# Kernel tuning notes

Measured on AMD Instinct MI355X. Metric: run time of the kernel, lower is better.

The kernel has to match this reference:

```python
import jax, jax.numpy as jnp
import numpy as np

HIDDEN = 1024
HEADS = 16
HEAD_DIM = HIDDEN // HEADS


def setup_inputs() -> dict:
    key = jax.random.key(0)
    k_x, k_wq, k_bq, k_wo, k_bo = jax.random.split(key, 5)
    x = jax.random.normal(k_x, (2, 2048, HIDDEN), dtype=jnp.float32)
    s = 1.0 / np.sqrt(HIDDEN)
    W_qkv = jax.random.uniform(k_wq, (HIDDEN, 3 * HIDDEN), jnp.float32, -s, s)
    b_qkv = jax.random.uniform(k_bq, (3 * HIDDEN,), jnp.float32, -s, s)
    W_out = jax.random.uniform(k_wo, (HIDDEN, HIDDEN), jnp.float32, -s, s)
    b_out = jax.random.uniform(k_bo, (HIDDEN,), jnp.float32, -s, s)
    return {"x": x, "W_qkv": W_qkv, "b_qkv": b_qkv, "W_out": W_out, "b_out": b_out}


def reference(x, W_qkv, b_qkv, W_out, b_out):
    B, S, D = x.shape
    qkv = x @ W_qkv + b_qkv                       # [B,S,3D]
    qkv = qkv.reshape(B, S, 3, HEADS, HEAD_DIM)
    qkv = jnp.transpose(qkv, (2, 0, 3, 1, 4))     # [3,B,H,S,Dh]
    q, k, v = qkv[0], qkv[1], qkv[2]
    scores = jnp.einsum("bhsd,bhtd->bhst", q, k) / np.sqrt(HEAD_DIM)
    attn = jax.nn.softmax(scores, axis=-1)        # [B,H,S,S]
    out = jnp.einsum("bhst,bhtd->bhsd", attn, v)  # [B,H,S,Dh]
    out = jnp.transpose(out, (0, 2, 1, 3)).reshape(B, S, D)
    return out @ W_out + b_out
```

## Files before the change

kernel.cpp:

```cpp
#include <hip/hip_runtime.h>
#include <hip/hip_bf16.h>

typedef short short8 __attribute__((ext_vector_type(8)));
typedef float float4_ __attribute__((ext_vector_type(4)));
typedef unsigned short ushort_t;
typedef unsigned int uint32_t_;
typedef uint32_t_ uint2v __attribute__((ext_vector_type(2)));
typedef uint32_t_ uint4v __attribute__((ext_vector_type(4)));

#define SCL 0.1803368801111f

__device__ __forceinline__ ushort_t f2bf(float f) {
    uint32_t_ u = __builtin_bit_cast(uint32_t_, f);
    u = (u + 0x7fffu + ((u >> 16) & 1u)) >> 16;
    return (ushort_t)u;
}

__device__ __forceinline__ uint32_t_ pack_bf16(float a, float b) {
    uint32_t_ ua = __builtin_bit_cast(uint32_t_, a) + 0x8000u;
    uint32_t_ ub = __builtin_bit_cast(uint32_t_, b) + 0x8000u;
    return __builtin_amdgcn_perm(ub, ua, 0x07060302);
}

__device__ __forceinline__ uint32_t_ cvt_pk_bf16(float lo, float hi) {
    uint32_t_ r;
    asm("v_cvt_pk_bf16_f32 %0, %1, %2" : "=v"(r) : "v"(lo), "v"(hi));
    return r;
}

#define MFMA32(a, b, c) __builtin_amdgcn_mfma_f32_16x16x32_bf16(a, b, c, 0, 0, 0)

#define GLD_LDS16(g, l) __builtin_amdgcn_global_load_lds( \
    (const __attribute__((address_space(1))) void*)(g),   \
    (__attribute__((address_space(3))) void*)(l), 16, 0, 0)

__global__ __launch_bounds__(256)
void prep_k(const float* __restrict__ x, ushort_t* __restrict__ x_bf,
            const float* __restrict__ Wqkv, ushort_t* __restrict__ WqkvT,
            const float* __restrict__ Wout, ushort_t* __restrict__ WoutT) {
    __shared__ float tile[32][33];
    const int id = blockIdx.x;
    const int tid = threadIdx.x;
    if (id < 4096) {
        int i = (id * 256 + tid) * 4;
        float4 v = *(const float4*)(x + i);
        uint32_t_ lo = (uint32_t_)f2bf(v.x) | ((uint32_t_)f2bf(v.y) << 16);
        uint32_t_ hi = (uint32_t_)f2bf(v.z) | ((uint32_t_)f2bf(v.w) << 16);
        *(uint2*)(x_bf + i) = make_uint2(lo, hi);
        return;
    }
    const float* in;
    ushort_t* out;
    int N, K, n0, k0;
    if (id < 7168) {
        int t = id - 4096;
        in = Wqkv; out = WqkvT; N = 3072; K = 1024;
        n0 = (t % 96) * 32; k0 = (t / 96) * 32;
    } else {
        int t = id - 7168;
        in = Wout; out = WoutT; N = 1024; K = 1024;
        n0 = (t & 31) * 32; k0 = (t >> 5) * 32;
    }
    int tx = tid & 31, ty = tid >> 5;
    #pragma unroll
    for (int i = 0; i < 32; i += 8)
        tile[ty + i][tx] = in[(size_t)(k0 + ty + i) * N + n0 + tx];
    __syncthreads();
    #pragma unroll
    for (int i = 0; i < 32; i += 8)
        out[(size_t)(n0 + ty + i) * K + k0 + tx] = f2bf(tile[tx][ty + i]);
}

template <int TN, bool QKV_EPI>
__global__ __launch_bounds__(256, TN == 128 ? 3 : 4)
void gemm_dbuf_k(const ushort_t* __restrict__ A, const ushort_t* __restrict__ Bt,
                 const float* __restrict__ bias, void* __restrict__ C,
                 ushort_t* __restrict__ Vt_out, int M, int N, int K) {
    constexpr int NB   = TN / 32;
    constexpr int SETB = 8192 + TN * 64;
    __shared__ char smem[2 * SETB];
    const int tid  = threadIdx.x;
    const int m0   = blockIdx.y * 128;
    const int n0   = blockIdx.x * TN;
    const int w    = tid >> 6;
    const int lane = tid & 63;
    const int wm   = (w >> 1) * 64;
    const int wn   = (w & 1) * (TN / 2);
    const int quad = lane >> 4;
    const int l16  = lane & 15;

    const int sr = 16 * w + (lane >> 2);
    const int sc = ((lane & 3) ^ ((sr >> 1) & 3)) * 8;
    const ushort_t* ag0 = A  + (size_t)(m0 + sr) * K + sc;
    const ushort_t* ag1 = A  + (size_t)(m0 + sr + 64) * K + sc;
    const ushort_t* bg0 = Bt + (size_t)(n0 + sr) * K + sc;
    const ushort_t* bg1 = Bt + (size_t)(n0 + sr + 64) * K + sc;
    char* sA = smem + 1024 * w;
    char* sB = smem + 8192 + 1024 * w;

    int aoff[4], boff[NB];
    #pragma unroll
    for (int i = 0; i < 4; i++) {
        int row = wm + i * 16 + l16;
        aoff[i] = row * 64 + ((quad ^ ((row >> 1) & 3)) * 16);
    }
    #pragma unroll
    for (int i = 0; i < NB; i++) {
        int row = wn + i * 16 + l16;
        boff[i] = 8192 + row * 64 + ((quad ^ ((row >> 1) & 3)) * 16);
    }

    float4_ acc[4][NB] = {};
    const int NIT = K >> 5;

    GLD_LDS16(ag0, sA);
    GLD_LDS16(ag1, sA + 4096);
    GLD_LDS16(bg0, sB);
    if (TN == 128) GLD_LDS16(bg1, sB + 4096);

    for (int it = 0; it < NIT; ++it) {
        __syncthreads();
        if (it + 1 < NIT) {
            const int nk = (it + 1) * 32;
            char* dA = sA + ((it + 1) & 1) * SETB;
            char* dB = sB + ((it + 1) & 1) * SETB;
            GLD_LDS16(ag0 + nk, dA);
            GLD_LDS16(ag1 + nk, dA + 4096);
            GLD_LDS16(bg0 + nk, dB);
            if (TN == 128) GLD_LDS16(bg1 + nk, dB + 4096);
        }
        const char* base = smem + (it & 1) * SETB;
        short8 af[4], bf[NB];
        #pragma unroll
        for (int i = 0; i < 4; i++)  af[i] = *(const short8*)(base + aoff[i]);
        #pragma unroll
        for (int i = 0; i < NB; i++) bf[i] = *(const short8*)(base + boff[i]);
        #pragma unroll
        for (int mi = 0; mi < 4; mi++)
            #pragma unroll
            for (int ni = 0; ni < NB; ni++)
                acc[mi][ni] = MFMA32(af[mi], bf[ni], acc[mi][ni]);
    }

    #pragma unroll
    for (int mi = 0; mi < 4; mi++) {
        int row = m0 + wm + mi * 16 + quad * 4;
        #pragma unroll
        for (int ni = 0; ni < NB; ni++) {
            int col = n0 + wn + ni * 16 + l16;
            float bb = bias[col];
            if (QKV_EPI) {
                if (col < 2048) {
                    float sc2 = (col < 1024) ? SCL : 1.0f;
                    #pragma unroll
                    for (int r = 0; r < 4; r++)
                        ((ushort_t*)C)[(size_t)(row + r) * 2048 + col] =
                            f2bf((acc[mi][ni][r] + bb) * sc2);
                } else {
                    int s0v  = row & 2047;
                    int spos = (s0v & ~31) | (quad << 3) | ((mi & 1) << 2);
                    size_t vrow = (size_t)((row >> 11) * 1024 + (col - 2048));
                    float v0 = acc[mi][ni][0] + bb, v1 = acc[mi][ni][1] + bb;
                    float v2 = acc[mi][ni][2] + bb, v3 = acc[mi][ni][3] + bb;
                    uint2v pk;
                    pk.x = pack_bf16(v0, v1);
                    pk.y = pack_bf16(v2, v3);
                    *(uint2v*)(Vt_out + vrow * 2048 + spos) = pk;
                }
            } else {
                #pragma unroll
                for (int r = 0; r < 4; r++)
                    ((float*)C)[(size_t)(row + r) * N + col] = acc[mi][ni][r] + bb;
            }
        }
    }
}

__global__ __launch_bounds__(256, 4)
void flash_attn_k(const ushort_t* __restrict__ qk, const ushort_t* __restrict__ vt,
                  ushort_t* __restrict__ out) {
    __shared__ char smem[32768];
    const int bh = blockIdx.x;
    const int b  = bh >> 4, h = bh & 15;
    const int q0 = blockIdx.y * 64;
    const int tid  = threadIdx.x;
    const int w    = tid >> 6;
    const int lane = tid & 63;
    const int quad = lane >> 4;
    const int l16  = lane & 15;
    const int qh   = w >> 1;
    const int kh   = w & 1;
    const size_t tok0 = (size_t)b * 2048;
    const int hq = h * 64;

    const int r0 = 16 * w + (lane >> 3), r1 = r0 + 8;
    const int s7 = lane & 7;
    const int c0 = (s7 ^ ((r0 >> 1) & 7)) * 8;
    const int c1 = (s7 ^ ((r1 >> 1) & 7)) * 8;
    const ushort_t* qg0 = qk + (tok0 + q0 + r0) * 2048 + hq + c0;
    const ushort_t* qg1 = qk + (tok0 + q0 + r1) * 2048 + hq + c1;
    const ushort_t* kg0 = qk + (tok0 + r0) * 2048 + 1024 + hq + c0;
    const ushort_t* kg1 = qk + (tok0 + r1) * 2048 + 1024 + hq + c1;
    const ushort_t* vg0 = vt + (size_t)(bh * 64 + r0) * 2048 + c0;
    const ushort_t* vg1 = vt + (size_t)(bh * 64 + r1) * 2048 + c1;
    char* stK = smem + 2048 * w;
    char* stV = smem + 8192 + 2048 * w;
    char* stQ = smem + 16384 + 2048 * w;

    GLD_LDS16(qg0, stQ);
    GLD_LDS16(qg1, stQ + 1024);
    GLD_LDS16(kg0, stK);
    GLD_LDS16(kg1, stK + 1024);
    GLD_LDS16(vg0, stV);
    GLD_LDS16(vg1, stV + 1024);
    __syncthreads();

    const int sw = (l16 >> 1) & 7;
    short8 qf[2][2];
    #pragma unroll
    for (int sub = 0; sub < 2; sub++)
        #pragma unroll
        for (int kk = 0; kk < 2; kk++) {
            int row = qh * 32 + sub * 16 + l16;
            qf[sub][kk] = *(const short8*)(smem + 16384 + row * 128 +
                                           (((kk * 4 + quad) ^ sw) * 16));
        }

    int koff[2][2], voff[4];
    #pragma unroll
    for (int mi = 0; mi < 2; mi++)
        #pragma unroll
        for (int kk = 0; kk < 2; kk++) {
            int row = kh * 32 + mi * 16 + l16;
            koff[mi][kk] = row * 128 + (((kk * 4 + quad) ^ sw) * 16);
        }
    #pragma unroll
    for (int di = 0; di < 4; di++) {
        int row = di * 16 + l16;
        voff[di] = 8192 + row * 128 + (((kh * 4 + quad) ^ sw) * 16);
    }

    float4_ ot[2][4] = {};
    float lsum[2] = {0.f, 0.f};
    short8 vprev[4];
    short8 bpprev[2];

    {
        __syncthreads();
        GLD_LDS16(kg0 + (size_t)64 * 2048, stK + 16384);
        GLD_LDS16(kg1 + (size_t)64 * 2048, stK + 16384 + 1024);
        GLD_LDS16(vg0 + 64, stV + 16384);
        GLD_LDS16(vg1 + 64, stV + 16384 + 1024);
        const char* base = smem;
        float4_ st[2][2];
        #pragma unroll
        for (int mi = 0; mi < 2; mi++) {
            short8 kf0 = *(const short8*)(base + koff[mi][0]);
            short8 kf1 = *(const short8*)(base + koff[mi][1]);
            #pragma unroll
            for (int sub = 0; sub < 2; sub++) {
                float4_ z = {0.f, 0.f, 0.f, 0.f};
                z = MFMA32(kf0, qf[sub][0], z);
                z = MFMA32(kf1, qf[sub][1], z);
                st[mi][sub] = z;
            }
        }
        #pragma unroll
        for (int di = 0; di < 4; di++)
            vprev[di] = *(const short8*)(base + voff[di]);
        #pragma unroll
        for (int sub = 0; sub < 2; sub++) {
            uint4v u;
            #pragma unroll
            for (int mi = 0; mi < 2; mi++) {
                float p0 = __builtin_amdgcn_exp2f(st[mi][sub][0]);
                float p1 = __builtin_amdgcn_exp2f(st[mi][sub][1]);
                float p2 = __builtin_amdgcn_exp2f(st[mi][sub][2]);
                float p3 = __builtin_amdgcn_exp2f(st[mi][sub][3]);
                lsum[sub] += (p0 + p1) + (p2 + p3);
                if (mi == 0) { u.x = cvt_pk_bf16(p0, p1); u.y = cvt_pk_bf16(p2, p3); }
                else         { u.z = cvt_pk_bf16(p0, p1); u.w = cvt_pk_bf16(p2, p3); }
            }
            bpprev[sub] = __builtin_bit_cast(short8, u);
        }
    }

    for (int kt = 64; kt < 2048; kt += 64) {
        __syncthreads();
        const int set = (kt >> 6) & 1;
        if (kt + 64 < 2048) {
            const int nb = (set ^ 1) * 16384;
            const size_t go = (size_t)(kt + 64);
            GLD_LDS16(kg0 + go * 2048, stK + nb);
            GLD_LDS16(kg1 + go * 2048, stK + nb + 1024);
            GLD_LDS16(vg0 + go, stV + nb);
            GLD_LDS16(vg1 + go, stV + nb + 1024);
        }
        const char* base = smem + set * 16384;

        float4_ st[2][2];
        #pragma unroll
        for (int mi = 0; mi < 2; mi++) {
            short8 kf0 = *(const short8*)(base + koff[mi][0]);
            short8 kf1 = *(const short8*)(base + koff[mi][1]);
            #pragma unroll
            for (int sub = 0; sub < 2; sub++) {
                float4_ z = {0.f, 0.f, 0.f, 0.f};
                z = MFMA32(kf0, qf[sub][0], z);
                z = MFMA32(kf1, qf[sub][1], z);
                st[mi][sub] = z;
            }
        }

        #pragma unroll
        for (int di = 0; di < 4; di++)
            #pragma unroll
            for (int sub = 0; sub < 2; sub++)
                ot[sub][di] = MFMA32(vprev[di], bpprev[sub], ot[sub][di]);

        #pragma unroll
        for (int di = 0; di < 4; di++)
            vprev[di] = *(const short8*)(base + voff[di]);

        #pragma unroll
        for (int sub = 0; sub < 2; sub++) {
            uint4v u;
            #pragma unroll
            for (int mi = 0; mi < 2; mi++) {
                float p0 = __builtin_amdgcn_exp2f(st[mi][sub][0]);
                float p1 = __builtin_amdgcn_exp2f(st[mi][sub][1]);
                float p2 = __builtin_amdgcn_exp2f(st[mi][sub][2]);
                float p3 = __builtin_amdgcn_exp2f(st[mi][sub][3]);
                lsum[sub] += (p0 + p1) + (p2 + p3);
                if (mi == 0) { u.x = cvt_pk_bf16(p0, p1); u.y = cvt_pk_bf16(p2, p3); }
                else         { u.z = cvt_pk_bf16(p0, p1); u.w = cvt_pk_bf16(p2, p3); }
            }
            bpprev[sub] = __builtin_bit_cast(short8, u);
        }
    }

    #pragma unroll
    for (int di = 0; di < 4; di++)
        #pragma unroll
        for (int sub = 0; sub < 2; sub++)
            ot[sub][di] = MFMA32(vprev[di], bpprev[sub], ot[sub][di]);

    #pragma unroll
    for (int sub = 0; sub < 2; sub++) {
        float t = lsum[sub];
        t += __shfl_xor(t, 16, 64);
        t += __shfl_xor(t, 32, 64);
        lsum[sub] = t;
    }

    float* Obuf = (float*)smem;
    float* lbuf = (float*)(smem + 17408);
    __syncthreads();
    #pragma unroll
    for (int sub = 0; sub < 2; sub++)
        lbuf[(qh * 32 + sub * 16 + l16) * 2 + kh] = lsum[sub];
    if (kh == 1) {
        #pragma unroll
        for (int sub = 0; sub < 2; sub++)
            #pragma unroll
            for (int di = 0; di < 4; di++)
                *(float4_*)&Obuf[(qh * 32 + sub * 16 + l16) * 68 + di * 16 + quad * 4] = ot[sub][di];
    }
    __syncthreads();
    if (kh == 0) {
        #pragma unroll
        for (int sub = 0; sub < 2; sub++)
            #pragma unroll
            for (int di = 0; di < 4; di++) {
                float4_* p = (float4_*)&Obuf[(qh * 32 + sub * 16 + l16) * 68 + di * 16 + quad * 4];
                *p = *p + ot[sub][di];
            }
    }
    __syncthreads();

    {
        int q  = tid >> 2;
        int ds = (tid & 3) * 16;
        float linv = 1.0f / (lbuf[q * 2] + lbuf[q * 2 + 1]);
        const float* ob = &Obuf[q * 68 + ds];
        float4_ v0 = *(const float4_*)(ob);
        float4_ v1 = *(const float4_*)(ob + 4);
        float4_ v2 = *(const float4_*)(ob + 8);
        float4_ v3 = *(const float4_*)(ob + 12);
        uint4v d0, d1;
        d0.x = pack_bf16(v0[0] * linv, v0[1] * linv);
        d0.y = pack_bf16(v0[2] * linv, v0[3] * linv);
        d0.z = pack_bf16(v1[0] * linv, v1[1] * linv);
        d0.w = pack_bf16(v1[2] * linv, v1[3] * linv);
        d1.x = pack_bf16(v2[0] * linv, v2[1] * linv);
        d1.y = pack_bf16(v2[2] * linv, v2[3] * linv);
        d1.z = pack_bf16(v3[0] * linv, v3[1] * linv);
        d1.w = pack_bf16(v3[2] * linv, v3[3] * linv);
        ushort_t* dst = out + (tok0 + q0 + (size_t)q) * 1024 + hq + ds;
        *(uint4v*)(dst)     = d0;
        *(uint4v*)(dst + 8) = d1;
    }
}

extern "C" void kernel_launch(void* const* d_in, const int* in_sizes, int n_in,
                              void* d_out, int out_size, void* d_ws, size_t ws_size,
                              hipStream_t stream) {
    const float* x    = (const float*)d_in[0];
    const float* Wqkv = (const float*)d_in[1];
    const float* bqkv = (const float*)d_in[2];
    const float* Wout = (const float*)d_in[3];
    const float* bout = (const float*)d_in[4];
    float* out = (float*)d_out;

    char* ws = (char*)d_ws;
    ushort_t* x_bf    = (ushort_t*)(ws);
    ushort_t* WqkvT   = (ushort_t*)(ws + 8388608);
    ushort_t* WoutT   = (ushort_t*)(ws + 14680064);
    ushort_t* qk_bf   = (ushort_t*)(ws + 16777216);
    ushort_t* vt_bf   = (ushort_t*)(ws + 33554432);
    ushort_t* attn_bf = (ushort_t*)(ws + 41943040);

    prep_k<<<8192, 256, 0, stream>>>(x, x_bf, Wqkv, WqkvT, Wout, WoutT);

    gemm_dbuf_k<128, true><<<dim3(24, 32), 256, 0, stream>>>(
        x_bf, WqkvT, bqkv, (void*)qk_bf, vt_bf, 4096, 3072, 1024);

    flash_attn_k<<<dim3(32, 32), 256, 0, stream>>>(qk_bf, vt_bf, attn_bf);

    gemm_dbuf_k<64, false><<<dim3(16, 32), 256, 0, stream>>>(
        attn_bf, WoutT, bout, (void*)out, nullptr, 4096, 1024, 1024);
}
```

Before: 176.3 us.

## Double flash-attention query tile to 128 rows with 512 threads; remap GEMM block order

The attention kernel now runs 8 waves per block over 128 query rows, so each K/V tile staged in shared memory is reused by twice as many queries and each thread issues one K and one V load per tile instead of two. Shared memory grows to 48KB and the grid halves. Separately, the GEMM kernels remap workgroup IDs in chunks of eight, likely to spread neighbouring tiles across XCDs for better L2 locality. Risks are lower occupancy per CU and fewer blocks for load balancing.

```diff
diff --git a/kernel.cpp b/kernel.cpp
--- a/kernel.cpp
+++ b/kernel.cpp
@@ -80,8 +80,11 @@
     constexpr int SETB = 8192 + TN * 64;
     __shared__ char smem[2 * SETB];
     const int tid  = threadIdx.x;
-    const int m0   = blockIdx.y * 128;
-    const int n0   = blockIdx.x * TN;
+    const int nwg = gridDim.x * gridDim.y;
+    const int id  = blockIdx.y * gridDim.x + blockIdx.x;
+    const int sid = (id & 7) * (nwg >> 3) + (id >> 3);
+    const int m0  = (sid / gridDim.x) * 128;
+    const int n0  = (sid % gridDim.x) * TN;
     const int w    = tid >> 6;
     const int lane = tid & 63;
     const int wm   = (w >> 1) * 64;
@@ -176,13 +179,13 @@
     }
 }
 
-__global__ __launch_bounds__(256, 4)
+__global__ __launch_bounds__(512, 4)
 void flash_attn_k(const ushort_t* __restrict__ qk, const ushort_t* __restrict__ vt,
                   ushort_t* __restrict__ out) {
-    __shared__ char smem[32768];
+    __shared__ char smem[49152];
     const int bh = blockIdx.x;
     const int b  = bh >> 4, h = bh & 15;
-    const int q0 = blockIdx.y * 64;
+    const int q0 = blockIdx.y * 128;
     const int tid  = threadIdx.x;
     const int w    = tid >> 6;
     const int lane = tid & 63;
@@ -193,26 +196,24 @@
     const size_t tok0 = (size_t)b * 2048;
     const int hq = h * 64;
 
-    const int r0 = 16 * w + (lane >> 3), r1 = r0 + 8;
-    const int s7 = lane & 7;
-    const int c0 = (s7 ^ ((r0 >> 1) & 7)) * 8;
-    const int c1 = (s7 ^ ((r1 >> 1) & 7)) * 8;
-    const ushort_t* qg0 = qk + (tok0 + q0 + r0) * 2048 + hq + c0;
-    const ushort_t* qg1 = qk + (tok0 + q0 + r1) * 2048 + hq + c1;
-    const ushort_t* kg0 = qk + (tok0 + r0) * 2048 + 1024 + hq + c0;
-    const ushort_t* kg1 = qk + (tok0 + r1) * 2048 + 1024 + hq + c1;
-    const ushort_t* vg0 = vt + (size_t)(bh * 64 + r0) * 2048 + c0;
-    const ushort_t* vg1 = vt + (size_t)(bh * 64 + r1) * 2048 + c1;
-    char* stK = smem + 2048 * w;
-    char* stV = smem + 8192 + 2048 * w;
-    char* stQ = smem + 16384 + 2048 * w;
+    const int s7  = lane & 7;
+    const int rk  = 8 * w + (lane >> 3);
+    const int ck  = (s7 ^ ((rk >> 1) & 7)) * 8;
+    const int rq0 = 16 * w + (lane >> 3), rq1 = rq0 + 8;
+    const int cq0 = (s7 ^ ((rq0 >> 1) & 7)) * 8;
+    const int cq1 = (s7 ^ ((rq1 >> 1) & 7)) * 8;
+    const ushort_t* qg0 = qk + (tok0 + q0 + rq0) * 2048 + hq + cq0;
+    const ushort_t* qg1 = qk + (tok0 + q0 + rq1) * 2048 + hq + cq1;
+    const ushort_t* kg  = qk + (tok0 + rk) * 2048 + 1024 + hq + ck;
+    const ushort_t* vg  = vt + (size_t)(bh * 64 + rk) * 2048 + ck;
+    char* stK = smem + 1024 * w;
+    char* stV = smem + 8192 + 1024 * w;
+    char* stQ = smem + 32768 + 2048 * w;
 
     GLD_LDS16(qg0, stQ);
     GLD_LDS16(qg1, stQ + 1024);
-    GLD_LDS16(kg0, stK);
-    GLD_LDS16(kg1, stK + 1024);
-    GLD_LDS16(vg0, stV);
-    GLD_LDS16(vg1, stV + 1024);
+    GLD_LDS16(kg, stK);
+    GLD_LDS16(vg, stV);
     __syncthreads();
 
     const int sw = (l16 >> 1) & 7;
@@ -222,7 +223,7 @@
         #pragma unroll
         for (int kk = 0; kk < 2; kk++) {
             int row = qh * 32 + sub * 16 + l16;
-            qf[sub][kk] = *(const short8*)(smem + 16384 + row * 128 +
+            qf[sub][kk] = *(const short8*)(smem + 32768 + row * 128 +
                                            (((kk * 4 + quad) ^ sw) * 16));
         }
 
@@ -245,12 +246,15 @@
     short8 vprev[4];
     short8 bpprev[2];
 
+    const ushort_t* kp = kg + (size_t)64 * 2048;
+    const ushort_t* vp = vg + 64;
+
     {
         __syncthreads();
-        GLD_LDS16(kg0 + (size_t)64 * 2048, stK + 16384);
-        GLD_LDS16(kg1 + (size_t)64 * 2048, stK + 16384 + 1024);
-        GLD_LDS16(vg0 + 64, stV + 16384);
-        GLD_LDS16(vg1 + 64, stV + 16384 + 1024);
+        GLD_LDS16(kp, stK + 16384);
+        GLD_LDS16(vp, stV + 16384);
+        kp += (size_t)64 * 2048;
+        vp += 64;
         const char* base = smem;
         float4_ st[2][2];
         #pragma unroll
@@ -290,11 +294,10 @@
         const int set = (kt >> 6) & 1;
         if (kt + 64 < 2048) {
             const int nb = (set ^ 1) * 16384;
-            const size_t go = (size_t)(kt + 64);
-            GLD_LDS16(kg0 + go * 2048, stK + nb);
-            GLD_LDS16(kg1 + go * 2048, stK + nb + 1024);
-            GLD_LDS16(vg0 + go, stV + nb);
-            GLD_LDS16(vg1 + go, stV + nb + 1024);
+            GLD_LDS16(kp, stK + nb);
+            GLD_LDS16(vp, stV + nb);
+            kp += (size_t)64 * 2048;
+            vp += 64;
         }
         const char* base = smem + set * 16384;
 
@@ -354,7 +357,7 @@
     }
 
     float* Obuf = (float*)smem;
-    float* lbuf = (float*)(smem + 17408);
+    float* lbuf = (float*)(smem + 34816);
     __syncthreads();
     #pragma unroll
     for (int sub = 0; sub < 2; sub++)
@@ -425,7 +428,7 @@
     gemm_dbuf_k<128, true><<<dim3(24, 32), 256, 0, stream>>>(
         x_bf, WqkvT, bqkv, (void*)qk_bf, vt_bf, 4096, 3072, 1024);
 
-    flash_attn_k<<<dim3(32, 32), 256, 0, stream>>>(qk_bf, vt_bf, attn_bf);
+    flash_attn_k<<<dim3(32, 16), 512, 0, stream>>>(qk_bf, vt_bf, attn_bf);
 
     gemm_dbuf_k<64, false><<<dim3(16, 32), 256, 0, stream>>>(
         attn_bf, WoutT, bout, (void*)out, nullptr, 4096, 1024, 1024);
```

Measured after the change: 174.1 us. About the same (-1.2%).
